# Kernel tuning notes

Measured on AMD Instinct MI355X. Metric: run time of the kernel, lower is better.

The kernel has to match this reference:

```python
import jax, jax.numpy as jnp
import numpy as np

B, T = 8, 1024
C, H, K, FF, L = 512, 8, 64, 2048, 6
STATE, INP, NBINS, NACT, MAXT = 128, 128, 41, 16, 2048
EPS = 1e-5


def _ln(x, g, b):
    m = jnp.mean(x, axis=-1, keepdims=True)
    v = jnp.var(x, axis=-1, keepdims=True)
    return (x - m) / jnp.sqrt(v + EPS) * g + b


def setup_inputs() -> dict:
    key = jax.random.key(0)
    ks = jax.random.split(key, 24)
    s = 0.02
    d = {}
    d["obs"] = jax.random.normal(ks[0], (B, T, STATE), jnp.float32)
    d["action"] = jax.random.randint(ks[1], (B, T), 0, NACT)
    d["step"] = jax.random.randint(ks[2], (B, T), 0, MAXT)
    # embeddings / input projections
    d["W_obs"] = s * jax.random.normal(ks[3], (STATE, C), jnp.float32)
    d["b_obs"] = jnp.zeros((C,), jnp.float32)
    d["E_act"] = s * jax.random.normal(ks[4], (NACT, C), jnp.float32)
    d["W_traj"] = s * jax.random.normal(ks[5], (2 * C, C), jnp.float32)
    d["b_traj"] = jnp.zeros((C,), jnp.float32)
    d["E_time"] = s * jax.random.normal(ks[6], (MAXT, C), jnp.float32)
    # per-layer stacked params (scanned over leading L axis)
    d["Wq"] = s * jax.random.normal(ks[7], (L, H, C, K), jnp.float32)
    d["Wk"] = s * jax.random.normal(ks[8], (L, H, C, K), jnp.float32)
    d["Wv"] = s * jax.random.normal(ks[9], (L, H, C, K), jnp.float32)
    d["Wp"] = s * jax.random.normal(ks[10], (L, H * K, C), jnp.float32)
    d["bp"] = jnp.zeros((L, C), jnp.float32)
    d["W1"] = s * jax.random.normal(ks[11], (L, C, FF), jnp.float32)
    d["b1"] = jnp.zeros((L, FF), jnp.float32)
    d["W2"] = s * jax.random.normal(ks[12], (L, FF, C), jnp.float32)
    d["b2"] = jnp.zeros((L, C), jnp.float32)
    d["g1"] = jnp.ones((L, C), jnp.float32)
    d["be1"] = jnp.zeros((L, C), jnp.float32)
    d["g2"] = jnp.ones((L, C), jnp.float32)
    d["be2"] = jnp.zeros((L, C), jnp.float32)
    # final norm + heads
    d["gf"] = jnp.ones((C,), jnp.float32)
    d["bf"] = jnp.zeros((C,), jnp.float32)
    d["W_oh"] = s * jax.random.normal(ks[13], (C, INP), jnp.float32)
    d["b_oh"] = jnp.zeros((INP,), jnp.float32)
    d["W_rh"] = s * jax.random.normal(ks[14], (C, NBINS), jnp.float32)
    d["b_rh"] = jnp.zeros((NBINS,), jnp.float32)
    d["W_dh"] = s * jax.random.normal(ks[15], (C, 1), jnp.float32)
    d["b_dh"] = jnp.zeros((1,), jnp.float32)
    return d


def reference(obs, action, step, W_obs, b_obs, E_act, W_traj, b_traj, E_time,
              Wq, Wk, Wv, Wp, bp, W1, b1, W2, b2, g1, be1, g2, be2,
              gf, bf, W_oh, b_oh, W_rh, b_rh, W_dh, b_dh):
    Bc, Tc = obs.shape[0], obs.shape[1]
    obs_emb = obs @ W_obs + b_obs                      # [B,T,C]
    act_emb = E_act[action]                            # [B,T,C]
    token = jnp.concatenate([obs_emb, act_emb], -1) @ W_traj + b_traj
    x = token + E_time[step]                           # [B,T,C]

    causal = jnp.tril(jnp.ones((Tc, Tc), bool))        # [T,T]
    scale = 1.0 / jnp.sqrt(jnp.asarray(K, x.dtype))

    def block(x, p):
        wq, wk, wv, wp, bpl, w1, b1l, w2, b2l, ga, ba, gb, bb = p
        q = jnp.einsum('btc,hck->bhtk', x, wq)
        k = jnp.einsum('btc,hck->bhtk', x, wk)
        v = jnp.einsum('btc,hck->bhtk', x, wv)
        wei = jnp.einsum('bhtk,bhsk->bhts', q, k) * scale
        wei = jnp.where(causal, wei, -jnp.inf)
        att = jax.nn.softmax(wei, axis=-1)             # dropout off (eval)
        o = jnp.einsum('bhts,bhsk->bhtk', att, v)
        o = o.transpose(0, 2, 1, 3).reshape(Bc, Tc, H * K)  # head-wise concat
        y = o @ wp + bpl
        x = _ln(x + y, ga, ba)                         # post-norm, as in source
        y = jax.nn.relu(x @ w1 + b1l) @ w2 + b2l
        x = _ln(x + y, gb, bb)
        return x, None

    x, _ = jax.lax.scan(block, x, (Wq, Wk, Wv, Wp, bp, W1, b1, W2, b2, g1, be1, g2, be2))
    x = _ln(x, gf, bf)
    obs_logits = x @ W_oh + b_oh
    reward_logits = x @ W_rh + b_rh
    done_logits = x @ W_dh + b_dh
    return (obs_logits, reward_logits, done_logits)
```

## Files before the change

### kernel.cpp

```cpp
#include <hip/hip_runtime.h>
#include <hip/hip_bf16.h>


#define TSEQ 1024
#define BB   8
#define CDIM 512
#define HH   8
#define KHD  64
#define FFD  2048
#define LL   6
#define MROWS (BB*TSEQ)

typedef __hip_bfloat16 bf16;
typedef __attribute__((ext_vector_type(8))) short bf16x8;
typedef __attribute__((ext_vector_type(4))) short bf16x4;
typedef __attribute__((ext_vector_type(4))) float f32x4;

#define MFMA16K16(a,b,c) __builtin_amdgcn_mfma_f32_16x16x16bf16_1k(a,b,c,0,0,0)

static __device__ __forceinline__ short f2bf_bits(float x) {
    bf16 t = __float2bfloat16(x);
    return *reinterpret_cast<short*>(&t);
}
static __device__ __forceinline__ float bf2f(short b) {
    unsigned u = ((unsigned)(unsigned short)b) << 16;
    return __uint_as_float(u);
}

static __device__ __forceinline__ void gload_lds16(const bf16* g, short* l) {
    __builtin_amdgcn_global_load_lds(
        (__attribute__((address_space(1))) const void*)g,
        (__attribute__((address_space(3))) void*)l, 16, 0, 0);
}

struct PrepJob { const float* src; long dstOff; int nrows; int kd; int type; };
struct PrepArgs { PrepJob jobs[48]; };

__global__ void __launch_bounds__(256) prep_weights(PrepArgs args, bf16* __restrict__ wsb)
{
    PrepJob J = args.jobs[blockIdx.y];
    const int tilesK = (J.kd + 63) >> 6;
    const int tilesN = (J.nrows + 63) >> 6;
    const int t = blockIdx.x;
    if (t >= tilesK * tilesN) return;
    const int tn = t / tilesK, tk = t - tn * tilesK;
    const int n0 = tn << 6, k0 = tk << 6;

    __shared__ float tile[64][65];
    const int tid = threadIdx.x;
    const bool full = (J.type != 3) && (n0 + 64 <= J.nrows) && (k0 + 64 <= J.kd);

    if (full) {
        const int c4 = (tid & 15) * 4;
        const int r0 = tid >> 4;
#pragma unroll
        for (int i = 0; i < 4; ++i) {
            int kl = r0 + i * 16;
            int k = k0 + kl;
            const float* src;
            if (J.type == 0) src = J.src + (long)k * J.nrows + n0 + c4;
            else             src = J.src + ((long)(n0 >> 6) * J.kd + k) * 64 + c4;
            float4 v = *(const float4*)src;
            tile[kl][c4 + 0] = v.x; tile[kl][c4 + 1] = v.y;
            tile[kl][c4 + 2] = v.z; tile[kl][c4 + 3] = v.w;
        }
        __syncthreads();
        const int kq = (tid & 15) * 4;
        const int n1 = tid >> 4;
#pragma unroll
        for (int i = 0; i < 4; ++i) {
            int nl = n1 + i * 16;
            bf16x4 o;
#pragma unroll
            for (int j2 = 0; j2 < 4; ++j2) o[j2] = f2bf_bits(tile[kq + j2][nl]);
            *(bf16x4*)(wsb + J.dstOff + (long)(n0 + nl) * J.kd + k0 + kq) = o;
        }
    } else {
#pragma unroll
        for (int i = 0; i < 16; ++i) {
            int e = tid + i * 256;
            int kl = e >> 6, nl = e & 63;
            int k = k0 + kl, n = n0 + nl;
            float v = 0.f;
            if (J.type != 3 && k < J.kd && n < J.nrows) {
                if (J.type == 0) v = J.src[(long)k * J.nrows + n];
                else             v = J.src[((long)(n >> 6) * J.kd + k) * 64 + (n & 63)];
            }
            tile[kl][nl] = v;
        }
        __syncthreads();
#pragma unroll
        for (int i = 0; i < 16; ++i) {
            int e = tid + i * 256;
            int nl = e >> 6, kl = e & 63;
            int n = n0 + nl, k = k0 + kl;
            if (n < J.nrows && k < J.kd)
                wsb[J.dstOff + (long)n * J.kd + k] = __float2bfloat16(tile[kl][nl]);
        }
    }
}

__global__ void build_head_bias(const float* __restrict__ b_oh, const float* __restrict__ b_rh,
                                const float* __restrict__ b_dh, float* __restrict__ hb)
{
    int i = threadIdx.x;
    float v = 0.f;
    if (i < 128) v = b_oh[i];
    else if (i < 169) v = b_rh[i - 128];
    else if (i == 169) v = b_dh[0];
    hb[i] = v;
}

template<int TN, int BK, int OUTMODE, bool BIAS, bool RELU>
__global__ void __launch_bounds__(256) gemm_kernel(
    const bf16* __restrict__ A, const bf16* __restrict__ BT,
    void* __restrict__ Cout, const float* __restrict__ bias,
    int M, int N, int Kd)
{
    constexpr int NJ = TN / 32;
    constexpr int SL = BK / 8;
    constexpr int AI = (128 * BK) / (8 * 256);
    constexpr int BI = (TN  * BK) / (8 * 256);
    __shared__ short As[128 * BK];
    __shared__ short Bs[TN * BK];
    const int tid = threadIdx.x;
    const int lane = tid & 63;
    const int w = tid >> 6;
    const int wm = w >> 1, wn = w & 1;
    const int m0 = blockIdx.x * 128;
    const int n0 = blockIdx.y * TN;
    const int g = lane >> 4, lr = lane & 15;

    f32x4 acc[4][NJ] = {};

    for (int k0 = 0; k0 < Kd; k0 += BK) {
#pragma unroll
        for (int it = 0; it < AI; ++it) {
            int cbase = (w * AI + it) * 64;
            int c = cbase + lane;
            int row = c / SL, slot = c % SL;
            int ss = slot ^ (row & (SL - 1));
            gload_lds16(A + (size_t)(m0 + row) * Kd + k0 + ss * 8, As + cbase * 8);
        }
#pragma unroll
        for (int it = 0; it < BI; ++it) {
            int cbase = (w * BI + it) * 64;
            int c = cbase + lane;
            int row = c / SL, slot = c % SL;
            int ss = slot ^ (row & (SL - 1));
            gload_lds16(BT + (size_t)(n0 + row) * Kd + k0 + ss * 8, Bs + cbase * 8);
        }
        __syncthreads();
#pragma unroll
        for (int kk = 0; kk < BK; kk += 32) {
            bf16x8 af[4], bfr[NJ];
#pragma unroll
            for (int i = 0; i < 4; ++i) {
                int row = wm*64 + i*16 + lr;
                int ss = ((kk >> 3) + g) ^ (row & (SL - 1));
                af[i] = *(const bf16x8*)(As + row * BK + ss * 8);
            }
#pragma unroll
            for (int j = 0; j < NJ; ++j) {
                int row = wn*(TN/2) + j*16 + lr;
                int ss = ((kk >> 3) + g) ^ (row & (SL - 1));
                bfr[j] = *(const bf16x8*)(Bs + row * BK + ss * 8);
            }
#pragma unroll
            for (int i = 0; i < 4; ++i)
#pragma unroll
                for (int j = 0; j < NJ; ++j)
                    acc[i][j] = __builtin_amdgcn_mfma_f32_16x16x32_bf16(af[i], bfr[j], acc[i][j], 0, 0, 0);
        }
        __syncthreads();
    }

#pragma unroll
    for (int i = 0; i < 4; ++i) {
#pragma unroll
        for (int j = 0; j < NJ; ++j) {
            int col = n0 + wn*(TN/2) + j*16 + lr;
            float bv = 0.f;
            if (BIAS) bv = bias[col];
#pragma unroll
            for (int r = 0; r < 4; ++r) {
                int row = m0 + wm*64 + i*16 + g*4 + r;
                float v = acc[i][j][r] + bv;
                if (RELU) v = fmaxf(v, 0.f);
                if (OUTMODE == 1) {
                    ((bf16*)Cout)[(size_t)row * N + col] = __float2bfloat16(v);
                } else if (OUTMODE == 2) {
                    float* outf = (float*)Cout;
                    if (col < 128)      outf[(size_t)row * 128 + col] = v;
                    else if (col < 169) outf[1048576 + (size_t)row * 41 + (col - 128)] = v;
                    else if (col == 169) outf[1384448 + (size_t)row] = v;
                } else {
                    ((float*)Cout)[(size_t)row * N + col] = v;
                }
            }
        }
    }
}

__global__ void __launch_bounds__(256) attn_kernel(const bf16* __restrict__ qkv, bf16* __restrict__ o)
{
    const int bh = blockIdx.x;
    const int z  = blockIdx.y;
    const int b = bh >> 3, h = bh & 7;
    const int tid = threadIdx.x, lane = tid & 63, w = tid >> 6;
    const int g = lane >> 4, lr = lane & 15;
    const int qlo = z, qhi = 15 - z;
    const float SCL = 0.125f * 1.44269504089f;

    __shared__ short Ks[128][72];
    __shared__ short Vs[8192];

    const size_t base = (size_t)b * TSEQ * 1536;

    bf16x8 qfL[2], qfH[2];
#pragma unroll
    for (int kk = 0; kk < 2; ++kk) {
        qfL[kk] = *(const bf16x8*)(qkv + base + (size_t)(qlo*64 + w*16 + lr) * 1536 + h*64 + kk*32 + g*8);
        qfH[kk] = *(const bf16x8*)(qkv + base + (size_t)(qhi*64 + w*16 + lr) * 1536 + h*64 + kk*32 + g*8);
    }

    f32x4 accL[4] = {}, accH[4] = {};
    float mL = -1e30f, lL = 0.f, mH = -1e30f, lH = 0.f;

    const short* vtr = &Vs[lane * 4];

    auto proc = [&](const bf16x8* qf, f32x4* acc, float& m, float& l, int qt, int kt) {
        f32x4 st[8];
#pragma unroll
        for (int j = 0; j < 8; ++j) {
            st[j] = f32x4{0.f, 0.f, 0.f, 0.f};
#pragma unroll
            for (int kk = 0; kk < 2; ++kk) {
                bf16x8 af = *(const bf16x8*)(&Ks[j*16 + lr][kk*32 + g*8]);
                st[j] = __builtin_amdgcn_mfma_f32_16x16x32_bf16(af, qf[kk], st[j], 0, 0, 0);
            }
        }
        const int qg = qt*64 + w*16 + lr;
        const bool diag = (kt == (qt >> 1));
        float vmax = -1e30f;
#pragma unroll
        for (int j = 0; j < 8; ++j)
#pragma unroll
            for (int r = 0; r < 4; ++r) {
                float v = st[j][r] * SCL;
                if (diag && (kt*128 + j*16 + g*4 + r) > qg) v = -1e30f;
                st[j][r] = v;
                vmax = fmaxf(vmax, v);
            }
        vmax = fmaxf(vmax, __shfl_xor(vmax, 16));
        vmax = fmaxf(vmax, __shfl_xor(vmax, 32));
        if (!__all(vmax <= m + 8.f)) {
            float mn = fmaxf(m, vmax);
            float alpha = exp2f(m - mn);
            l *= alpha;
            float av[4];
#pragma unroll
            for (int r = 0; r < 4; ++r) av[r] = __shfl(alpha, g*4 + r);
#pragma unroll
            for (int dj = 0; dj < 4; ++dj)
#pragma unroll
                for (int r = 0; r < 4; ++r) acc[dj][r] *= av[r];
            m = mn;
        }
        float psum = 0.f;
        bf16x4 pf[8];
#pragma unroll
        for (int j = 0; j < 8; ++j)
#pragma unroll
            for (int r = 0; r < 4; ++r) {
                float p = exp2f(st[j][r] - m);
                psum += p;
                pf[j][r] = f2bf_bits(p);
            }
        psum += __shfl_xor(psum, 16);
        psum += __shfl_xor(psum, 32);
        l += psum;
#pragma unroll
        for (int half = 0; half < 4; ++half) {
            bf16x4 vf[2][4];
#pragma unroll
            for (int jj = 0; jj < 2; ++jj)
#pragma unroll
                for (int dj = 0; dj < 4; ++dj) {
                    asm volatile("ds_read_b64_tr_b16 %0, %1"
                        : "=v"(vf[jj][dj])
                        : "v"((const __attribute__((address_space(3))) short*)
                              (vtr + ((half*2 + jj)*4 + dj) * 256)));
                }
            asm volatile("s_waitcnt lgkmcnt(0)" ::: "memory");
            __builtin_amdgcn_sched_barrier(0);
#pragma unroll
            for (int jj = 0; jj < 2; ++jj)
#pragma unroll
                for (int dj = 0; dj < 4; ++dj)
                    acc[dj] = MFMA16K16(pf[half*2 + jj], vf[jj][dj], acc[dj]);
        }
    };

    const int ktmax = qhi >> 1;
    for (int kt = 0; kt <= ktmax; ++kt) {
#pragma unroll
        for (int it = 0; it < 4; ++it) {
            int idx = tid + it * 256;
            int row = idx >> 3;
            int col = (idx & 7) << 3;
            *(bf16x8*)(&Ks[row][col]) =
                *(const bf16x8*)(qkv + base + (size_t)(kt*128 + row)*1536 + 512 + h*64 + col);
            bf16x8 vv = *(const bf16x8*)(qkv + base + (size_t)(kt*128 + row)*1536 + 1024 + h*64 + col);
            int dst = ((row >> 4)*4 + (col >> 4))*256 + (row & 15)*16 + (col & 8);
            *(bf16x8*)(&Vs[dst]) = vv;
        }
        __syncthreads();
        proc(qfH, accH, mH, lH, qhi, kt);
        if (kt <= (qlo >> 1)) proc(qfL, accL, mL, lL, qlo, kt);
        __syncthreads();
    }

    auto wout = [&](const f32x4* acc, float l, int qt) {
        float linv = 1.f / l;
        float lv[4];
#pragma unroll
        for (int r = 0; r < 4; ++r) lv[r] = __shfl(linv, g*4 + r);
#pragma unroll
        for (int dj = 0; dj < 4; ++dj)
#pragma unroll
            for (int r = 0; r < 4; ++r) {
                int trow = qt*64 + w*16 + g*4 + r;
                o[((size_t)(b*TSEQ + trow))*512 + h*64 + dj*16 + lr] =
                    __float2bfloat16(acc[dj][r] * lv[r]);
            }
    };
    wout(accH, lH, qhi);
    wout(accL, lL, qlo);
}

template<bool HAS_RES, bool WRITE_F32, bool YBF16>
__global__ void __launch_bounds__(256) ln_kernel(
    const void* __restrict__ y_, const float* __restrict__ xin,
    float* __restrict__ xout, bf16* __restrict__ xb,
    const float* __restrict__ gamma, const float* __restrict__ beta)
{
    int row = blockIdx.x * 4 + (threadIdx.x >> 6);
    int lane = threadIdx.x & 63;
    int c0 = lane * 8;
    size_t rb = (size_t)row * CDIM + c0;
    float u[8];
    if (YBF16) {
        bf16x8 yv = *(const bf16x8*)((const bf16*)y_ + rb);
#pragma unroll
        for (int i = 0; i < 8; ++i) u[i] = bf2f(yv[i]);
    } else {
        float4 a = *(const float4*)((const float*)y_ + rb);
        float4 b2 = *(const float4*)((const float*)y_ + rb + 4);
        u[0]=a.x; u[1]=a.y; u[2]=a.z; u[3]=a.w;
        u[4]=b2.x; u[5]=b2.y; u[6]=b2.z; u[7]=b2.w;
    }
    if (HAS_RES) {
        float4 a = *(const float4*)(xin + rb);
        float4 b2 = *(const float4*)(xin + rb + 4);
        u[0]+=a.x; u[1]+=a.y; u[2]+=a.z; u[3]+=a.w;
        u[4]+=b2.x; u[5]+=b2.y; u[6]+=b2.z; u[7]+=b2.w;
    }
    float s = 0.f, sq = 0.f;
#pragma unroll
    for (int i = 0; i < 8; ++i) { s += u[i]; sq += u[i]*u[i]; }
#pragma unroll
    for (int off = 1; off < 64; off <<= 1) { s += __shfl_xor(s, off); sq += __shfl_xor(sq, off); }
    float mean = s * (1.f / 512.f);
    float var  = sq * (1.f / 512.f) - mean * mean;
    float rstd = rsqrtf(var + 1e-5f);
    float4 g0 = *(const float4*)(gamma + c0);
    float4 g1 = *(const float4*)(gamma + c0 + 4);
    float4 be0 = *(const float4*)(beta + c0);
    float4 be1v = *(const float4*)(beta + c0 + 4);
    float gv[8] = {g0.x,g0.y,g0.z,g0.w,g1.x,g1.y,g1.z,g1.w};
    float bv[8] = {be0.x,be0.y,be0.z,be0.w,be1v.x,be1v.y,be1v.z,be1v.w};
    float o8[8];
    bf16x8 ob;
#pragma unroll
    for (int i = 0; i < 8; ++i) {
        o8[i] = (u[i] - mean) * rstd * gv[i] + bv[i];
        ob[i] = f2bf_bits(o8[i]);
    }
    if (WRITE_F32) {
        *(float4*)(xout + rb)     = float4{o8[0],o8[1],o8[2],o8[3]};
        *(float4*)(xout + rb + 4) = float4{o8[4],o8[5],o8[6],o8[7]};
    }
    *(bf16x8*)(xb + rb) = ob;
}

__global__ void __launch_bounds__(256) obs_convert(const float* __restrict__ obs, bf16* __restrict__ out)
{
    int idx = (blockIdx.x * 256 + threadIdx.x) * 4;
    float4 v = *(const float4*)(obs + idx);
    bf16x4 o = { f2bf_bits(v.x), f2bf_bits(v.y), f2bf_bits(v.z), f2bf_bits(v.w) };
    *(bf16x4*)(out + idx) = o;
}

__global__ void __launch_bounds__(256) concat_kernel(
    const float* __restrict__ obs_emb, const int* __restrict__ action,
    const float* __restrict__ E_act, bf16* __restrict__ cc)
{
    int row = blockIdx.x;
    int a = action[row];
    int c = threadIdx.x * 4;
    float4 v = (c < 512) ? *(const float4*)(obs_emb + (size_t)row * 512 + c)
                         : *(const float4*)(E_act + (size_t)a * 512 + (c - 512));
    bf16x4 o = { f2bf_bits(v.x), f2bf_bits(v.y), f2bf_bits(v.z), f2bf_bits(v.w) };
    *(bf16x4*)(cc + (size_t)row * 1024 + c) = o;
}

__global__ void __launch_bounds__(256) xinit_kernel(
    float* __restrict__ x, const int* __restrict__ step,
    const float* __restrict__ E_time, bf16* __restrict__ xb)
{
    int row = blockIdx.x * 2 + (threadIdx.x >> 7);
    int c = (threadIdx.x & 127) * 4;
    int st = step[row];
    float4 xv = *(const float4*)(x + (size_t)row * 512 + c);
    float4 tv = *(const float4*)(E_time + (size_t)st * 512 + c);
    float4 v = {xv.x + tv.x, xv.y + tv.y, xv.z + tv.z, xv.w + tv.w};
    *(float4*)(x + (size_t)row * 512 + c) = v;
    bf16x4 o = { f2bf_bits(v.x), f2bf_bits(v.y), f2bf_bits(v.z), f2bf_bits(v.w) };
    *(bf16x4*)(xb + (size_t)row * 512 + c) = o;
}

extern "C" void kernel_launch(void* const* d_in, const int* in_sizes, int n_in,
                              void* d_out, int out_size, void* d_ws, size_t ws_size,
                              hipStream_t stream)
{
    const float* obs    = (const float*)d_in[0];
    const int*   action = (const int*)  d_in[1];
    const int*   step   = (const int*)  d_in[2];
    const float* W_obs  = (const float*)d_in[3];
    const float* b_obs  = (const float*)d_in[4];
    const float* E_act  = (const float*)d_in[5];
    const float* W_traj = (const float*)d_in[6];
    const float* b_traj = (const float*)d_in[7];
    const float* E_time = (const float*)d_in[8];
    const float* Wq  = (const float*)d_in[9];
    const float* Wk  = (const float*)d_in[10];
    const float* Wv  = (const float*)d_in[11];
    const float* Wp  = (const float*)d_in[12];
    const float* bp  = (const float*)d_in[13];
    const float* W1  = (const float*)d_in[14];
    const float* b1  = (const float*)d_in[15];
    const float* W2  = (const float*)d_in[16];
    const float* b2  = (const float*)d_in[17];
    const float* g1  = (const float*)d_in[18];
    const float* be1 = (const float*)d_in[19];
    const float* g2  = (const float*)d_in[20];
    const float* be2 = (const float*)d_in[21];
    const float* gf  = (const float*)d_in[22];
    const float* bfp = (const float*)d_in[23];
    const float* W_oh = (const float*)d_in[24];
    const float* b_oh = (const float*)d_in[25];
    const float* W_rh = (const float*)d_in[26];
    const float* b_rh = (const float*)d_in[27];
    const float* W_dh = (const float*)d_in[28];
    const float* b_dh = (const float*)d_in[29];

    char* ws  = (char*)d_ws;
    bf16* wsb = (bf16*)ws;

    long off = 0;
    const long oWT_obs  = off; off += 512L * 128;
    const long oWT_traj = off; off += 512L * 1024;
    const long oWT_qkv  = off; off += 6L * 1536 * 512;
    const long oWT_p    = off; off += 6L * 512 * 512;
    const long oWT_1    = off; off += 6L * 2048 * 512;
    const long oWT_2    = off; off += 6L * 512 * 2048;
    const long oWT_hd   = off; off += 256L * 512;
    size_t byteOff = ((size_t)off * 2 + 255) & ~(size_t)255;

    auto take = [&](size_t bytes) {
        void* p = ws + byteOff;
        byteOff = (byteOff + bytes + 255) & ~(size_t)255;
        return p;
    };
    float* head_bias = (float*)take(256 * 4);
    bf16*  xb   = (bf16*) take((size_t)MROWS * 512 * 2);
    float* x    = (float*)take((size_t)MROWS * 512 * 4);
    float* y    = (float*)take((size_t)MROWS * 512 * 4);
    bf16*  qkv  = (bf16*) take((size_t)MROWS * 1536 * 2);
    bf16*  o    = (bf16*) take((size_t)MROWS * 512 * 2);
    bf16*  hbuf = (bf16*) take((size_t)MROWS * 2048 * 2);
    (void)ws_size; (void)in_sizes; (void)n_in; (void)out_size;

    PrepArgs pa;
    int nj = 0;
    auto addJob = [&](const float* src, long dstOff, int nrows, int kd, int type) {
        pa.jobs[nj].src = src; pa.jobs[nj].dstOff = dstOff;
        pa.jobs[nj].nrows = nrows; pa.jobs[nj].kd = kd; pa.jobs[nj].type = type; ++nj;
    };
    addJob(W_obs,  oWT_obs,  512, 128,  0);
    addJob(W_traj, oWT_traj, 512, 1024, 0);
    for (int l = 0; l < 6; ++l) {
        long qb = oWT_qkv + (long)l * 1536 * 512;
        addJob(Wq + (long)l * 8 * 512 * 64, qb,               512, 512, 1);
        addJob(Wk + (long)l * 8 * 512 * 64, qb + 512L * 512,  512, 512, 1);
        addJob(Wv + (long)l * 8 * 512 * 64, qb + 1024L * 512, 512, 512, 1);
        addJob(Wp + (long)l * 512 * 512,  oWT_p + (long)l * 512 * 512,  512,  512,  0);
        addJob(W1 + (long)l * 512 * 2048, oWT_1 + (long)l * 2048 * 512, 2048, 512,  0);
        addJob(W2 + (long)l * 2048 * 512, oWT_2 + (long)l * 512 * 2048, 512,  2048, 0);
    }
    addJob(W_oh, oWT_hd,             128, 512, 0);
    addJob(W_rh, oWT_hd + 128L*512,  41,  512, 0);
    addJob(W_dh, oWT_hd + 169L*512,  1,   512, 0);
    addJob(nullptr, oWT_hd + 170L*512, 86, 512, 3);

    prep_weights<<<dim3(256, nj), 256, 0, stream>>>(pa, wsb);
    build_head_bias<<<1, 256, 0, stream>>>(b_oh, b_rh, b_dh, head_bias);

    bf16* obs_bf = o;
    obs_convert<<<(MROWS * 128) / 1024, 256, 0, stream>>>(obs, obs_bf);
    gemm_kernel<64, 128, 0, true, false><<<dim3(64, 8), 256, 0, stream>>>(
        obs_bf, wsb + oWT_obs, y, b_obs, MROWS, 512, 128);
    bf16* cc = hbuf;
    concat_kernel<<<MROWS, 256, 0, stream>>>(y, action, E_act, cc);
    gemm_kernel<64, 128, 0, true, false><<<dim3(64, 8), 256, 0, stream>>>(
        cc, wsb + oWT_traj, x, b_traj, MROWS, 512, 1024);
    xinit_kernel<<<MROWS / 2, 256, 0, stream>>>(x, step, E_time, xb);

    for (int l = 0; l < 6; ++l) {
        gemm_kernel<128, 64, 1, false, false><<<dim3(64, 12), 256, 0, stream>>>(
            xb, wsb + oWT_qkv + (long)l * 1536 * 512, qkv, nullptr, MROWS, 1536, 512);
        attn_kernel<<<dim3(64, 8), 256, 0, stream>>>(qkv, o);
        gemm_kernel<64, 128, 1, true, false><<<dim3(64, 8), 256, 0, stream>>>(
            o, wsb + oWT_p + (long)l * 512 * 512, hbuf, bp + (long)l * 512, MROWS, 512, 512);
        ln_kernel<true, true, true><<<MROWS / 4, 256, 0, stream>>>(
            hbuf, x, x, xb, g1 + l * 512, be1 + l * 512);
        gemm_kernel<128, 64, 1, true, true><<<dim3(64, 16), 256, 0, stream>>>(
            xb, wsb + oWT_1 + (long)l * 2048 * 512, hbuf, b1 + l * 2048, MROWS, 2048, 512);
        gemm_kernel<64, 128, 1, true, false><<<dim3(64, 8), 256, 0, stream>>>(
            hbuf, wsb + oWT_2 + (long)l * 512 * 2048, o, b2 + l * 512, MROWS, 512, 2048);
        ln_kernel<true, true, true><<<MROWS / 4, 256, 0, stream>>>(
            o, x, x, xb, g2 + l * 512, be2 + l * 512);
    }

    ln_kernel<false, false, false><<<MROWS / 4, 256, 0, stream>>>(
        x, nullptr, nullptr, xb, gf, bfp);
    gemm_kernel<64, 128, 2, true, false><<<dim3(64, 4), 256, 0, stream>>>(
        xb, wsb + oWT_hd, d_out, head_bias, MROWS, 256, 512);
}
```

Measured before the change: 866.3 us.

## Widen weight-prep tiles, raise MFMA wave priority, emit obs embedding in bf16

The weight-prep kernel now transposes 64x128 tiles and writes 16-byte bf16x8 stores, halving the grid. The attention kernel wraps its MFMA blocks in s_setprio so waves issuing matrix ops get scheduling priority. The observation embedding GEMM writes bf16 directly into a scratch buffer, so the concat kernel copies bf16 instead of reading fp32 and converting. This trades larger LDS use in prep and a bf16 rounding of the obs embedding for less memory traffic and possibly better MFMA issue overlap.

```diff
diff --git a/kernel.cpp b/kernel.cpp
--- a/kernel.cpp
+++ b/kernel.cpp
@@ -39,22 +39,22 @@
 __global__ void __launch_bounds__(256) prep_weights(PrepArgs args, bf16* __restrict__ wsb)
 {
     PrepJob J = args.jobs[blockIdx.y];
-    const int tilesK = (J.kd + 63) >> 6;
+    const int tilesK = (J.kd + 127) >> 7;
     const int tilesN = (J.nrows + 63) >> 6;
     const int t = blockIdx.x;
     if (t >= tilesK * tilesN) return;
     const int tn = t / tilesK, tk = t - tn * tilesK;
-    const int n0 = tn << 6, k0 = tk << 6;
-
-    __shared__ float tile[64][65];
+    const int n0 = tn << 6, k0 = tk << 7;
+
+    __shared__ float tile[128][65];
     const int tid = threadIdx.x;
-    const bool full = (J.type != 3) && (n0 + 64 <= J.nrows) && (k0 + 64 <= J.kd);
+    const bool full = (J.type != 3) && (n0 + 64 <= J.nrows) && (k0 + 128 <= J.kd);
 
     if (full) {
         const int c4 = (tid & 15) * 4;
         const int r0 = tid >> 4;
 #pragma unroll
-        for (int i = 0; i < 4; ++i) {
+        for (int i = 0; i < 8; ++i) {
             int kl = r0 + i * 16;
             int k = k0 + kl;
             const float* src;
@@ -65,19 +65,19 @@
             tile[kl][c4 + 2] = v.z; tile[kl][c4 + 3] = v.w;
         }
         __syncthreads();
-        const int kq = (tid & 15) * 4;
+        const int kq = (tid & 15) * 8;
         const int n1 = tid >> 4;
 #pragma unroll
         for (int i = 0; i < 4; ++i) {
             int nl = n1 + i * 16;
-            bf16x4 o;
-#pragma unroll
-            for (int j2 = 0; j2 < 4; ++j2) o[j2] = f2bf_bits(tile[kq + j2][nl]);
-            *(bf16x4*)(wsb + J.dstOff + (long)(n0 + nl) * J.kd + k0 + kq) = o;
+            bf16x8 o;
+#pragma unroll
+            for (int j2 = 0; j2 < 8; ++j2) o[j2] = f2bf_bits(tile[kq + j2][nl]);
+            *(bf16x8*)(wsb + J.dstOff + (long)(n0 + nl) * J.kd + k0 + kq) = o;
         }
     } else {
 #pragma unroll
-        for (int i = 0; i < 16; ++i) {
+        for (int i = 0; i < 32; ++i) {
             int e = tid + i * 256;
             int kl = e >> 6, nl = e & 63;
             int k = k0 + kl, n = n0 + nl;
@@ -90,12 +90,16 @@
         }
         __syncthreads();
 #pragma unroll
-        for (int i = 0; i < 16; ++i) {
+        for (int i = 0; i < 32; ++i) {
             int e = tid + i * 256;
-            int nl = e >> 6, kl = e & 63;
-            int n = n0 + nl, k = k0 + kl;
-            if (n < J.nrows && k < J.kd)
-                wsb[J.dstOff + (long)n * J.kd + k] = __float2bfloat16(tile[kl][nl]);
+            int nl = e >> 6;
+            int kl = e & 63;
+            int e2 = tid + i * 256;
+            int n = n0 + (e2 >> 7);
+            int k = k0 + (e2 & 127);
+            if ((e2 >> 7) < 64 && n < J.nrows && k < J.kd)
+                wsb[J.dstOff + (long)n * J.kd + k] = __float2bfloat16(tile[e2 & 127][e2 >> 7]);
+            (void)nl; (void)kl;
         }
     }
 }
@@ -231,6 +235,7 @@
 
     auto proc = [&](const bf16x8* qf, f32x4* acc, float& m, float& l, int qt, int kt) {
         f32x4 st[8];
+        __builtin_amdgcn_s_setprio(1);
 #pragma unroll
         for (int j = 0; j < 8; ++j) {
             st[j] = f32x4{0.f, 0.f, 0.f, 0.f};
@@ -240,6 +245,7 @@
                 st[j] = __builtin_amdgcn_mfma_f32_16x16x32_bf16(af, qf[kk], st[j], 0, 0, 0);
             }
         }
+        __builtin_amdgcn_s_setprio(0);
         const int qg = qt*64 + w*16 + lr;
         const bool diag = (kt == (qt >> 1));
         float vmax = -1e30f;
@@ -294,11 +300,13 @@
                 }
             asm volatile("s_waitcnt lgkmcnt(0)" ::: "memory");
             __builtin_amdgcn_sched_barrier(0);
+            __builtin_amdgcn_s_setprio(1);
 #pragma unroll
             for (int jj = 0; jj < 2; ++jj)
 #pragma unroll
                 for (int dj = 0; dj < 4; ++dj)
                     acc[dj] = MFMA16K16(pf[half*2 + jj], vf[jj][dj], acc[dj]);
+            __builtin_amdgcn_s_setprio(0);
         }
     };
 
@@ -403,16 +411,20 @@
 }
 
 __global__ void __launch_bounds__(256) concat_kernel(
-    const float* __restrict__ obs_emb, const int* __restrict__ action,
+    const bf16* __restrict__ obs_emb, const int* __restrict__ action,
     const float* __restrict__ E_act, bf16* __restrict__ cc)
 {
     int row = blockIdx.x;
     int a = action[row];
     int c = threadIdx.x * 4;
-    float4 v = (c < 512) ? *(const float4*)(obs_emb + (size_t)row * 512 + c)
-                         : *(const float4*)(E_act + (size_t)a * 512 + (c - 512));
-    bf16x4 o = { f2bf_bits(v.x), f2bf_bits(v.y), f2bf_bits(v.z), f2bf_bits(v.w) };
-    *(bf16x4*)(cc + (size_t)row * 1024 + c) = o;
+    if (c < 512) {
+        *(bf16x4*)(cc + (size_t)row * 1024 + c) =
+            *(const bf16x4*)(obs_emb + (size_t)row * 512 + c);
+    } else {
+        float4 v = *(const float4*)(E_act + (size_t)a * 512 + (c - 512));
+        bf16x4 o = { f2bf_bits(v.x), f2bf_bits(v.y), f2bf_bits(v.z), f2bf_bits(v.w) };
+        *(bf16x4*)(cc + (size_t)row * 1024 + c) = o;
+    }
 }
 
 __global__ void __launch_bounds__(256) xinit_kernel(
@@ -490,7 +502,7 @@
     bf16*  qkv  = (bf16*) take((size_t)MROWS * 1536 * 2);
     bf16*  o    = (bf16*) take((size_t)MROWS * 512 * 2);
     bf16*  hbuf = (bf16*) take((size_t)MROWS * 2048 * 2);
-    (void)ws_size; (void)in_sizes; (void)n_in; (void)out_size;
+    (void)ws_size; (void)in_sizes; (void)n_in; (void)out_size; (void)y;
 
     PrepArgs pa;
     int nj = 0;
@@ -514,15 +526,16 @@
     addJob(W_dh, oWT_hd + 169L*512,  1,   512, 0);
     addJob(nullptr, oWT_hd + 170L*512, 86, 512, 3);
 
-    prep_weights<<<dim3(256, nj), 256, 0, stream>>>(pa, wsb);
+    prep_weights<<<dim3(128, nj), 256, 0, stream>>>(pa, wsb);
     build_head_bias<<<1, 256, 0, stream>>>(b_oh, b_rh, b_dh, head_bias);
 
     bf16* obs_bf = o;
     obs_convert<<<(MROWS * 128) / 1024, 256, 0, stream>>>(obs, obs_bf);
-    gemm_kernel<64, 128, 0, true, false><<<dim3(64, 8), 256, 0, stream>>>(
-        obs_bf, wsb + oWT_obs, y, b_obs, MROWS, 512, 128);
+    bf16* obs_emb = qkv;
+    gemm_kernel<64, 128, 1, true, false><<<dim3(64, 8), 256, 0, stream>>>(
+        obs_bf, wsb + oWT_obs, obs_emb, b_obs, MROWS, 512, 128);
     bf16* cc = hbuf;
-    concat_kernel<<<MROWS, 256, 0, stream>>>(y, action, E_act, cc);
+    concat_kernel<<<MROWS, 256, 0, stream>>>(obs_emb, action, E_act, cc);
     gemm_kernel<64, 128, 0, true, false><<<dim3(64, 8), 256, 0, stream>>>(
         cc, wsb + oWT_traj, x, b_traj, MROWS, 512, 1024);
     xinit_kernel<<<MROWS / 2, 256, 0, stream>>>(x, step, E_time, xb);
```

Measured after the change: 866.3 us. Within noise of the previous version (+0.0%).
